# Kernel optimization log

Hardware: AMD Instinct MI355X
Metric: run time of the kernel (lower is better)

The kernel has to match this reference:

```python
import jax, jax.numpy as jnp
import numpy as np

H = 1024
NUM_HEADS = 16
HEAD_DIM = H // NUM_HEADS
EPS = 1e-6
GEN_E, GEN_IE = 8, 4096 // 8     # general experts, per-expert intermediate
MOD_E, MOD_IE = 4, 4096 // 4     # per-modality experts, per-expert intermediate


def layernorm(x, g, b):
    m = jnp.mean(x, axis=-1, keepdims=True)
    v = jnp.mean((x - m) ** 2, axis=-1, keepdims=True)
    return (x - m) * jax.lax.rsqrt(v + EPS) * g + b


def attention(x, qkv_w, qkv_b, proj_w, proj_b):
    B, N, _ = x.shape
    qkv = (x @ qkv_w + qkv_b).reshape(B, N, 3, NUM_HEADS, HEAD_DIM)
    qkv = jnp.transpose(qkv, (2, 0, 3, 1, 4))  # [3,B,h,N,d]
    q, k, v = qkv[0], qkv[1], qkv[2]
    scale = HEAD_DIM ** -0.5
    attn = jax.nn.softmax(jnp.einsum('bhnd,bhmd->bhnm', q, k) * scale, axis=-1)
    out = jnp.einsum('bhnm,bhmd->bhnd', attn, v)
    out = jnp.transpose(out, (0, 2, 1, 3)).reshape(B, N, H)
    return out @ proj_w + proj_b


def routed_mlp(x, position_ids, gate_up, down, ie):
    # expert_id = position % num_experts; compute all experts then select per token
    # (avoids materializing per-token [T,H,2I] gathered weights).
    E = gate_up.shape[0]
    eids = position_ids % E  # [B,N]
    gu = jnp.einsum('bnh,ehi->bnei', x, gate_up)              # [B,N,E,2*ie]
    gu = jnp.take_along_axis(gu, eids[..., None, None], axis=2)[:, :, 0]
    gate, up = gu[..., :ie], gu[..., ie:]
    inter = jax.nn.silu(gate) * up                             # [B,N,ie]
    dn = jnp.einsum('bni,eih->bneh', inter, down)              # [B,N,E,H]
    return jnp.take_along_axis(dn, eids[..., None, None], axis=2)[:, :, 0]


def setup_inputs() -> dict:
    key = jax.random.key(0)
    ks = jax.random.split(key, 16)
    B, N = 2, 2048
    inp = {
        'x': jax.random.normal(ks[0], (B, N, H), jnp.float32),
        'qkv_w': jax.random.normal(ks[1], (H, 3 * H), jnp.float32) * 0.02,
        'qkv_b': jnp.zeros((3 * H,), jnp.float32),
        'proj_w': jax.random.normal(ks[2], (H, H), jnp.float32) * 0.02,
        'proj_b': jnp.zeros((H,), jnp.float32),
        'ln1_g': jnp.ones((H,), jnp.float32), 'ln1_b': jnp.zeros((H,), jnp.float32),
        'ln2_g': jnp.ones((H,), jnp.float32), 'ln2_b': jnp.zeros((H,), jnp.float32),
        'ln3_g': jnp.ones((H,), jnp.float32), 'ln3_b': jnp.zeros((H,), jnp.float32),
        'gen_gu': jax.random.normal(ks[3], (GEN_E, H, 2 * GEN_IE), jnp.float32) * 0.02,
        'gen_dn': jax.random.normal(ks[4], (GEN_E, GEN_IE, H), jnp.float32) * 0.02,
        'text_gu': jax.random.normal(ks[5], (MOD_E, H, 2 * MOD_IE), jnp.float32) * 0.02,
        'text_dn': jax.random.normal(ks[6], (MOD_E, MOD_IE, H), jnp.float32) * 0.02,
        'img_gu': jax.random.normal(ks[7], (MOD_E, H, 2 * MOD_IE), jnp.float32) * 0.02,
        'img_dn': jax.random.normal(ks[8], (MOD_E, MOD_IE, H), jnp.float32) * 0.02,
        'aud_gu': jax.random.normal(ks[9], (MOD_E, H, 2 * MOD_IE), jnp.float32) * 0.02,
        'aud_dn': jax.random.normal(ks[10], (MOD_E, MOD_IE, H), jnp.float32) * 0.02,
        'vid_gu': jax.random.normal(ks[11], (MOD_E, H, 2 * MOD_IE), jnp.float32) * 0.02,
        'vid_dn': jax.random.normal(ks[12], (MOD_E, MOD_IE, H), jnp.float32) * 0.02,
        'modality_ids': jax.random.randint(ks[13], (B, N), 0, 4, jnp.int32),
        'position_ids': jnp.arange(B * N, dtype=jnp.int32).reshape(B, N),
    }
    return inp


def reference(x, qkv_w, qkv_b, proj_w, proj_b,
              ln1_g, ln1_b, ln2_g, ln2_b, ln3_g, ln3_b,
              gen_gu, gen_dn, text_gu, text_dn, img_gu, img_dn,
              aud_gu, aud_dn, vid_gu, vid_dn,
              modality_ids, position_ids):
    x = x + attention(layernorm(x, ln1_g, ln1_b), qkv_w, qkv_b, proj_w, proj_b)
    x = x + routed_mlp(layernorm(x, ln2_g, ln2_b), position_ids, gen_gu, gen_dn, GEN_IE)
    normed = layernorm(x, ln3_g, ln3_b)
    tm = (modality_ids == 0)[..., None].astype(x.dtype)
    im = (modality_ids == 1)[..., None].astype(x.dtype)
    am = (modality_ids == 2)[..., None].astype(x.dtype)
    vm = (modality_ids == 3)[..., None].astype(x.dtype)
    x = x + (routed_mlp(normed, position_ids, text_gu, text_dn, MOD_IE) * tm
             + routed_mlp(normed, position_ids, img_gu, img_dn, MOD_IE) * im
             + routed_mlp(normed, position_ids, aud_gu, aud_dn, MOD_IE) * am
             + routed_mlp(normed, position_ids, vid_gu, vid_dn, MOD_IE) * vm)
    return x
```

## Files before the change

kernel.cpp:

```cpp
#include <hip/hip_runtime.h>

#define T_TOKENS 4096
#define HDIM 1024

typedef __attribute__((ext_vector_type(8))) short bf16x8;
typedef __attribute__((ext_vector_type(4))) float f32x4;

#define EXP2F(x) __builtin_amdgcn_exp2f(x)

static __device__ inline unsigned short f2bf(float f) {
  unsigned u = __float_as_uint(f);
  unsigned r = (u + 0x7FFFu + ((u >> 16) & 1u)) >> 16;
  return (unsigned short)r;
}
static __device__ __forceinline__ unsigned cvtpk(float lo, float hi) {
  unsigned r;
  asm("v_cvt_pk_bf16_f32 %0, %1, %2" : "=v"(r) : "v"(lo), "v"(hi));
  return r;
}
static __device__ __forceinline__ void gl16(const void* g, void* l) {
  __builtin_amdgcn_global_load_lds((const __attribute__((address_space(1))) void*)g,
                                   (__attribute__((address_space(3))) void*)l, 16, 0, 0);
}

__launch_bounds__(256)
__global__ void ln_kernel(const float* __restrict__ in, const float* __restrict__ g,
                          const float* __restrict__ b, unsigned short* __restrict__ out) {
  const int row = blockIdx.x;
  const int tid = threadIdx.x;
  const long base = (long)row * HDIM;
  float4 v = *(const float4*)(in + base + tid * 4);
  __shared__ float red[256];
  red[tid] = v.x + v.y + v.z + v.w;
  __syncthreads();
  for (int st = 128; st > 0; st >>= 1) {
    if (tid < st) red[tid] += red[tid + st];
    __syncthreads();
  }
  const float mean = red[0] * (1.f / HDIM);
  __syncthreads();
  const float dx = v.x - mean, dy = v.y - mean, dz = v.z - mean, dw = v.w - mean;
  red[tid] = dx * dx + dy * dy + dz * dz + dw * dw;
  __syncthreads();
  for (int st = 128; st > 0; st >>= 1) {
    if (tid < st) red[tid] += red[tid + st];
    __syncthreads();
  }
  const float rstd = rsqrtf(red[0] * (1.f / HDIM) + 1e-6f);
  const int c = tid * 4;
  const float4 g4 = *(const float4*)(g + c);
  const float4 b4 = *(const float4*)(b + c);
  uint2 o;
  o.x = cvtpk(dx * rstd * g4.x + b4.x, dy * rstd * g4.y + b4.y);
  o.y = cvtpk(dz * rstd * g4.z + b4.z, dw * rstd * g4.w + b4.w);
  *(uint2*)(out + base + c) = o;
}

__launch_bounds__(256)
__global__ void build_groups(const int* __restrict__ pids, const int* __restrict__ mids,
                             int* __restrict__ gen_cnt, int* __restrict__ gen_list,
                             int* __restrict__ mod_cnt, int* __restrict__ mod_list) {
  const int t = blockIdx.x * 256 + threadIdx.x;
  if (t >= T_TOKENS) return;
  const int p = pids[t];
  const int ge = p & 7;
  int s = atomicAdd(&gen_cnt[ge], 1);
  if (s < 512) gen_list[ge * 512 + s] = t;
  const int g = mids[t] * 4 + (p & 3);
  s = atomicAdd(&mod_cnt[g], 1);
  if (s < 1024) mod_list[g * 1024 + s] = t;
}

__launch_bounds__(256)
__global__ void convert_w(const float* __restrict__ W, unsigned short* __restrict__ Wt,
                          int K, int N) {
  const long zo = (long)blockIdx.z * K * N;
  const float* Wp = W + zo;
  unsigned short* Wo = Wt + zo;
  const int n0 = blockIdx.x * 64, k0 = blockIdx.y * 64;
  __shared__ float T[64][65];
  const int tid = threadIdx.x;
#pragma unroll
  for (int i = 0; i < 4; ++i) {
    const int item = tid + i * 256;
    const int kk = item >> 4, c4 = (item & 15) * 4;
    const float4 v = *(const float4*)(Wp + (long)(k0 + kk) * N + n0 + c4);
    T[c4 + 0][kk] = v.x; T[c4 + 1][kk] = v.y; T[c4 + 2][kk] = v.z; T[c4 + 3][kk] = v.w;
  }
  __syncthreads();
#pragma unroll
  for (int i = 0; i < 4; ++i) {
    const int item = tid + i * 256;
    const int nn = item >> 4, k4 = (item & 15) * 4;
    uint2 p;
    p.x = cvtpk(T[nn][k4 + 0], T[nn][k4 + 1]);
    p.y = cvtpk(T[nn][k4 + 2], T[nn][k4 + 3]);
    *(uint2*)(Wo + (long)(n0 + nn) * K + k0 + k4) = p;
  }
}

enum { MODE_DENSE = 0, MODE_GEN = 1, MODE_MOD = 2 };
enum { OM_F32R = 0, OM_BF16 = 1, OM_QKV = 2 };

template <int MODE, int OMODE, bool WBF16, bool BIAS, int BM, int BN>
__launch_bounds__(256)
__global__ void mgemm(const unsigned short* __restrict__ A,
                      const void* __restrict__ w0, const float* __restrict__ w1,
                      const float* __restrict__ w2, const float* __restrict__ w3,
                      long wstep, const float* __restrict__ bias,
                      const float* __restrict__ resid, void* __restrict__ Cout,
                      unsigned short* __restrict__ qb, unsigned short* __restrict__ kb,
                      unsigned short* __restrict__ vtb,
                      int K, int N,
                      const int* __restrict__ cnts, const int* __restrict__ rowlist,
                      int cap) {
  const int z = blockIdx.z;
  const int n0 = blockIdx.x * BN;
  const int m0 = blockIdx.y * BM;

  int Meff = 1 << 30;
  const int* list = nullptr;
  if constexpr (MODE != MODE_DENSE) {
    Meff = cnts[z];
    if (m0 >= Meff) return;
    list = rowlist + z * cap;
  }

  constexpr int MR = BM / 32;
  constexpr int NR = BN / 32;
  constexpr int JB = BN / 32;
  constexpr int ABUF = BM * 128;
  constexpr int BBUF = BN * 128;
  __shared__ char As[2 * ABUF];
  __shared__ char Bs[2 * BBUF];

  const int tid = threadIdx.x;
  const int w = tid >> 6;
  const int lane = tid & 63;
  const int wm = w >> 1, wn = w & 1;
  const int srow = lane >> 3, sc = lane & 7;

  const unsigned short* asrc[MR];
#pragma unroll
  for (int i = 0; i < MR; ++i) {
    const int r = w * (BM / 4) + i * 8 + srow;
    long tok;
    if constexpr (MODE == MODE_DENSE) {
      tok = m0 + r;
    } else {
      int gm = m0 + r;
      if (gm >= Meff) gm = Meff - 1;
      tok = (long)list[gm];
    }
    asrc[i] = A + tok * (long)K + (sc ^ (r & 7)) * 8;
  }

  const unsigned short* bsrc[NR];
  const float* bptr[JB];
  int boff[JB];
  if constexpr (WBF16) {
    const unsigned short* W = (const unsigned short*)w0;
    if constexpr (MODE != MODE_DENSE) W += (long)z * wstep;
#pragma unroll
    for (int i = 0; i < NR; ++i) {
      const int r = w * (BN / 4) + i * 8 + srow;
      bsrc[i] = W + (long)(n0 + r) * K + (sc ^ (r & 7)) * 8;
    }
  } else {
    const float* W;
    if constexpr (MODE == MODE_MOD) {
      const int mm = z >> 2;
      const float* basep = (mm == 0) ? (const float*)w0 : (mm == 1) ? w1 : (mm == 2) ? w2 : w3;
      W = basep + (long)(z & 3) * wstep;
    } else {
      W = (const float*)w0 + (MODE != MODE_DENSE ? (long)z * wstep : 0);
    }
#pragma unroll
    for (int j = 0; j < JB; ++j) {
      const int item = tid + j * 256;
      const int kc = item / BN;
      const int nl = item % BN;
      bptr[j] = W + (long)(kc * 8) * N + n0 + nl;
      boff[j] = (nl * 128 + kc * 16) ^ ((nl & 7) << 4);
    }
  }

  f32x4 acc[MR][NR] = {};
  float kv[JB][8];

  auto stageA = [&](int s, int kt) {
#pragma unroll
    for (int i = 0; i < MR; ++i)
      gl16(asrc[i] + kt, As + s * ABUF + w * (BM * 32) + i * 1024);
  };
  auto stageB16 = [&](int s, int kt) {
#pragma unroll
    for (int i = 0; i < NR; ++i)
      gl16(bsrc[i] + kt, Bs + s * BBUF + w * (BN * 32) + i * 1024);
  };
  auto loadB = [&](int kt) {
#pragma unroll
    for (int j = 0; j < JB; ++j) {
      const float* bp = bptr[j] + (long)kt * N;
#pragma unroll
      for (int u = 0; u < 8; ++u) kv[j][u] = bp[(long)u * N];
    }
  };
  auto writeB = [&](int s) {
#pragma unroll
    for (int j = 0; j < JB; ++j) {
      uint4 p;
      p.x = cvtpk(kv[j][0], kv[j][1]);
      p.y = cvtpk(kv[j][2], kv[j][3]);
      p.z = cvtpk(kv[j][4], kv[j][5]);
      p.w = cvtpk(kv[j][6], kv[j][7]);
      *(uint4*)(Bs + s * BBUF + boff[j]) = p;
    }
  };
  auto compute = [&](int s) {
#pragma unroll
    for (int kk = 0; kk < 2; ++kk) {
      const int kb2 = kk * 64 + (lane >> 4) * 16;
      bf16x8 af[MR], bfr[NR];
#pragma unroll
      for (int f = 0; f < MR; ++f) {
        const int ar = wm * (BM / 2) + f * 16 + (lane & 15);
        af[f] = *(bf16x8*)(As + s * ABUF + ((ar * 128 + kb2) ^ ((ar & 7) << 4)));
      }
#pragma unroll
      for (int f = 0; f < NR; ++f) {
        const int br = wn * (BN / 2) + f * 16 + (lane & 15);
        bfr[f] = *(bf16x8*)(Bs + s * BBUF + ((br * 128 + kb2) ^ ((br & 7) << 4)));
      }
#pragma unroll
      for (int mf = 0; mf < MR; ++mf)
#pragma unroll
        for (int nf = 0; nf < NR; ++nf)
          acc[mf][nf] =
              __builtin_amdgcn_mfma_f32_16x16x32_bf16(af[mf], bfr[nf], acc[mf][nf], 0, 0, 0);
    }
  };

  const int nk = K >> 6;
  stageA(0, 0);
  if constexpr (WBF16) {
    stageB16(0, 0);
  } else {
    loadB(0);
    writeB(0);
  }
  __syncthreads();

  int sel = 0;
  for (int t = 0; t < nk; ++t) {
    const bool more = (t + 1) < nk;
    const int ktn = (t + 1) * 64;
    if (more) {
      stageA(sel ^ 1, ktn);
      if constexpr (WBF16) stageB16(sel ^ 1, ktn);
      else loadB(ktn);
    }
    compute(sel);
    if constexpr (!WBF16) {
      if (more) writeB(sel ^ 1);
    }
    __syncthreads();
    sel ^= 1;
  }

  const int lr4 = (lane >> 4) * 4;
  const int lc = lane & 15;
#pragma unroll
  for (int mf = 0; mf < MR; ++mf) {
#pragma unroll
    for (int r = 0; r < 4; ++r) {
      const int gm = m0 + wm * (BM / 2) + mf * 16 + lr4 + r;
      long orow;
      if constexpr (MODE == MODE_DENSE) {
        orow = gm;
      } else {
        if (gm >= Meff) continue;
        orow = (long)list[gm];
      }
#pragma unroll
      for (int nf = 0; nf < NR; ++nf) {
        const int gc = n0 + wn * (BN / 2) + nf * 16 + lc;
        float val = acc[mf][nf][r];
        if constexpr (BIAS) val += bias[gc];
        if constexpr (OMODE == OM_F32R) {
          val += resid[orow * (long)N + gc];
          ((float*)Cout)[orow * (long)N + gc] = val;
        } else if constexpr (OMODE == OM_BF16) {
          ((unsigned short*)Cout)[orow * (long)N + gc] = f2bf(val);
        } else {
          const int bb = (int)(orow >> 11), tl = (int)orow & 2047;
          const int seg = gc >> 10, hc = gc & 1023, h = hc >> 6, d = hc & 63;
          if (seg == 0)
            qb[(((long)(bb * 16 + h) * 2048) + tl) * 64 + d] = f2bf(val * 0.18033688011112042f);
          else if (seg == 1)
            kb[(((long)(bb * 16 + h) * 2048) + tl) * 64 + d] = f2bf(val);
          else
            vtb[((long)(bb * 16 + h) * 64 + d) * 2048 + tl] = f2bf(val);
        }
      }
    }
  }
}

__launch_bounds__(256)
__global__ void attn_kernel(const unsigned short* __restrict__ Qb,
                            const unsigned short* __restrict__ Kb,
                            const unsigned short* __restrict__ Vtb,
                            unsigned short* __restrict__ out) {
  const int lin = blockIdx.x + blockIdx.y * 32;
  const int xcd = lin & 7, rank = lin >> 3;
  const int bh = xcd * 4 + (rank >> 5);
  const int qt = rank & 31;
  const int b = bh >> 4, h = bh & 15;
  const int tid = threadIdx.x;
  const int w = tid >> 6;
  const int lane = tid & 63;
  const int g = lane >> 4;
  const int q = lane & 15;

  constexpr int PSTR = 272;
  __shared__ char Ksb[128 * 128];
  __shared__ char Vsb[64 * 256];
  __shared__ char Psb[4 * 16 * PSTR];
  char* Pwb = Psb + w * 16 * PSTR;

  const unsigned short* Qh = Qb + ((long)(b * 16 + h) * 2048 + qt * 64) * 64;
  const unsigned short* Kh = Kb + (long)(b * 16 + h) * 2048 * 64;
  const unsigned short* Vh = Vtb + (long)(b * 16 + h) * 64 * 2048;

  bf16x8 qf[2];
#pragma unroll
  for (int kst = 0; kst < 2; ++kst)
    qf[kst] = *(const bf16x8*)(Qh + (w * 16 + q) * 64 + kst * 32 + g * 8);

  const unsigned short* ksrc[4];
  const unsigned short* vsrc[4];
  char* kld = Ksb + w * 4096;
  char* vld = Vsb + w * 4096;
#pragma unroll
  for (int i = 0; i < 4; ++i) {
    const int r = w * 32 + i * 8 + (lane >> 3);
    ksrc[i] = Kh + (long)r * 64 + ((lane & 7) ^ (r & 7)) * 8;
    const int d = w * 16 + i * 4 + (lane >> 4);
    vsrc[i] = Vh + (long)d * 2048 + ((lane & 15) ^ (d & 7)) * 8;
  }

  float m_run = -1e30f, l_run = 0.f;
  f32x4 acc[4] = {};

  for (int kt = 0; kt < 16; ++kt) {
    __syncthreads();
#pragma unroll
    for (int i = 0; i < 4; ++i) gl16(ksrc[i] + (long)kt * 128 * 64, kld + i * 1024);
#pragma unroll
    for (int i = 0; i < 4; ++i) gl16(vsrc[i] + kt * 128, vld + i * 1024);
    __syncthreads();

    f32x4 sf[8];
#pragma unroll
    for (int f = 0; f < 8; ++f) {
      const int krow = f * 16 + q;
      const int sw = (krow & 7) << 4;
      const bf16x8 k0 = *(bf16x8*)(Ksb + krow * 128 + ((g * 16) ^ sw));
      const bf16x8 k1 = *(bf16x8*)(Ksb + krow * 128 + ((64 + g * 16) ^ sw));
      f32x4 t = {};
      t = __builtin_amdgcn_mfma_f32_16x16x32_bf16(k0, qf[0], t, 0, 0, 0);
      sf[f] = __builtin_amdgcn_mfma_f32_16x16x32_bf16(k1, qf[1], t, 0, 0, 0);
    }

    float pm = fmaxf(fmaxf(sf[0][0], sf[0][1]), fmaxf(sf[0][2], sf[0][3]));
#pragma unroll
    for (int f = 1; f < 8; ++f)
      pm = fmaxf(pm, fmaxf(fmaxf(sf[f][0], sf[f][1]), fmaxf(sf[f][2], sf[f][3])));
    pm = fmaxf(pm, __shfl_xor(pm, 16));
    pm = fmaxf(pm, __shfl_xor(pm, 32));
    float al = 1.f;
    if (!__all(pm - m_run <= 8.f)) {
      const float mn = fmaxf(m_run, pm);
      al = EXP2F(m_run - mn);
      m_run = mn;
#pragma unroll
      for (int r = 0; r < 4; ++r) {
        const float aO = __shfl(al, g * 4 + r, 64);
        acc[0][r] *= aO; acc[1][r] *= aO; acc[2][r] *= aO; acc[3][r] *= aO;
      }
    }

    float ls = 0.f;
#pragma unroll
    for (int f = 0; f < 8; ++f) {
#pragma unroll
      for (int r = 0; r < 4; ++r) sf[f][r] = EXP2F(sf[f][r] - m_run);
      ls += (sf[f][0] + sf[f][1]) + (sf[f][2] + sf[f][3]);
    }
    ls += __shfl_xor(ls, 16);
    ls += __shfl_xor(ls, 32);
    l_run = l_run * al + ls;

#pragma unroll
    for (int f = 0; f < 8; ++f) {
      const int base = q * PSTR + f * 32 + g * 8;
      *(unsigned*)(Pwb + base) = cvtpk(sf[f][0], sf[f][1]);
      *(unsigned*)(Pwb + base + 4) = cvtpk(sf[f][2], sf[f][3]);
    }

#pragma unroll
    for (int kst = 0; kst < 4; ++kst) {
      const bf16x8 pa = *(bf16x8*)(Pwb + q * PSTR + kst * 64 + g * 16);
#pragma unroll
      for (int df = 0; df < 4; ++df) {
        const int vrow = df * 16 + q;
        const int vsw = (vrow & 7) << 4;
        const bf16x8 vf = *(bf16x8*)(Vsb + vrow * 256 + ((kst * 64 + g * 16) ^ vsw));
        acc[df] = __builtin_amdgcn_mfma_f32_16x16x32_bf16(pa, vf, acc[df], 0, 0, 0);
      }
    }
  }

  float linv[4];
#pragma unroll
  for (int r = 0; r < 4; ++r) linv[r] = 1.f / __shfl(l_run, g * 4 + r, 64);
  unsigned short* op = out + (long)(b * 2048 + qt * 64 + w * 16) * 1024 + h * 64;
#pragma unroll
  for (int df = 0; df < 4; ++df)
#pragma unroll
    for (int r = 0; r < 4; ++r) {
      const int row = g * 4 + r;
      op[(long)row * 1024 + df * 16 + q] = f2bf(acc[df][r] * linv[r]);
    }
}

__launch_bounds__(256)
__global__ void silu_bf(const unsigned short* __restrict__ gu, unsigned short* __restrict__ inter,
                        int IE2, int IE, int shift) {
  const int total = T_TOKENS << shift;
  for (int idx = blockIdx.x * 256 + threadIdx.x; idx < total; idx += gridDim.x * 256) {
    const int t = idx >> shift;
    const int r8 = (idx & ((1 << shift) - 1)) * 8;
    const unsigned short* gp = gu + (long)t * IE2 + r8;
    const uint4 gg = *(const uint4*)gp;
    const uint4 uu = *(const uint4*)(gp + IE);
    const unsigned gw[4] = {gg.x, gg.y, gg.z, gg.w};
    const unsigned uw[4] = {uu.x, uu.y, uu.z, uu.w};
    uint4 o;
    unsigned ow[4];
#pragma unroll
    for (int qq = 0; qq < 4; ++qq) {
      const float g0 = __uint_as_float(gw[qq] << 16);
      const float g1 = __uint_as_float(gw[qq] & 0xffff0000u);
      const float u0 = __uint_as_float(uw[qq] << 16);
      const float u1 = __uint_as_float(uw[qq] & 0xffff0000u);
      const float r0 = g0 / (1.f + __expf(-g0)) * u0;
      const float r1 = g1 / (1.f + __expf(-g1)) * u1;
      ow[qq] = cvtpk(r0, r1);
    }
    o.x = ow[0]; o.y = ow[1]; o.z = ow[2]; o.w = ow[3];
    *(uint4*)(inter + (long)t * IE + r8) = o;
  }
}

extern "C" void kernel_launch(void* const* d_in, const int* in_sizes, int n_in,
                              void* d_out, int out_size, void* d_ws, size_t ws_size,
                              hipStream_t stream) {
  const float* x       = (const float*)d_in[0];
  const float* qkv_w   = (const float*)d_in[1];
  const float* qkv_b   = (const float*)d_in[2];
  const float* proj_w  = (const float*)d_in[3];
  const float* proj_b  = (const float*)d_in[4];
  const float* ln1_g   = (const float*)d_in[5];
  const float* ln1_b   = (const float*)d_in[6];
  const float* ln2_g   = (const float*)d_in[7];
  const float* ln2_b   = (const float*)d_in[8];
  const float* ln3_g   = (const float*)d_in[9];
  const float* ln3_b   = (const float*)d_in[10];
  const float* gen_gu  = (const float*)d_in[11];
  const float* gen_dn  = (const float*)d_in[12];
  const float* text_gu = (const float*)d_in[13];
  const float* text_dn = (const float*)d_in[14];
  const float* img_gu  = (const float*)d_in[15];
  const float* img_dn  = (const float*)d_in[16];
  const float* aud_gu  = (const float*)d_in[17];
  const float* aud_dn  = (const float*)d_in[18];
  const float* vid_gu  = (const float*)d_in[19];
  const float* vid_dn  = (const float*)d_in[20];
  const int* mids      = (const int*)d_in[21];
  const int* pids      = (const int*)d_in[22];
  float* out = (float*)d_out;
  char* ws = (char*)d_ws;

  const unsigned long MB = 1ul << 20;
  unsigned short* lnb   = (unsigned short*)(ws);
  unsigned short* Qb    = (unsigned short*)(ws + 8 * MB);
  unsigned short* Kb    = (unsigned short*)(ws + 16 * MB);
  unsigned short* Vtb   = (unsigned short*)(ws + 24 * MB);
  unsigned short* attno = (unsigned short*)(ws + 32 * MB);
  unsigned short* wqkv  = (unsigned short*)(ws + 40 * MB);
  unsigned short* wproj = (unsigned short*)(ws + 46 * MB);
  unsigned short* wggu  = (unsigned short*)(ws + 48 * MB);
  unsigned short* wgdn  = (unsigned short*)(ws + 64 * MB);
  int* gen_cnt  = (int*)(ws + 72 * MB);
  int* mod_cnt  = gen_cnt + 8;
  int* gen_list = gen_cnt + 32;
  int* mod_list = gen_list + 8 * 512;
  unsigned short* guo    = Qb;
  unsigned short* intero = Vtb;

  (void)hipMemsetAsync(gen_cnt, 0, (8 + 16) * sizeof(int), stream);
  build_groups<<<16, 256, 0, stream>>>(pids, mids, gen_cnt, gen_list, mod_cnt, mod_list);

  convert_w<<<dim3(48, 16, 1), 256, 0, stream>>>(qkv_w, wqkv, 1024, 3072);
  convert_w<<<dim3(16, 16, 1), 256, 0, stream>>>(proj_w, wproj, 1024, 1024);
  convert_w<<<dim3(16, 16, 8), 256, 0, stream>>>(gen_gu, wggu, 1024, 1024);
  convert_w<<<dim3(16, 8, 8), 256, 0, stream>>>(gen_dn, wgdn, 512, 1024);

  ln_kernel<<<4096, 256, 0, stream>>>(x, ln1_g, ln1_b, lnb);
  mgemm<MODE_DENSE, OM_QKV, true, true, 128, 128><<<dim3(24, 32, 1), 256, 0, stream>>>(
      lnb, wqkv, nullptr, nullptr, nullptr, 0L, qkv_b, nullptr, nullptr,
      Qb, Kb, Vtb, 1024, 3072, nullptr, nullptr, 0);
  attn_kernel<<<dim3(32, 32, 1), 256, 0, stream>>>(Qb, Kb, Vtb, attno);
  mgemm<MODE_DENSE, OM_F32R, true, true, 128, 128><<<dim3(8, 32, 1), 256, 0, stream>>>(
      attno, wproj, nullptr, nullptr, nullptr, 0L, proj_b, x, out,
      nullptr, nullptr, nullptr, 1024, 1024, nullptr, nullptr, 0);

  ln_kernel<<<4096, 256, 0, stream>>>(out, ln2_g, ln2_b, lnb);
  mgemm<MODE_GEN, OM_BF16, true, false, 128, 128><<<dim3(8, 4, 8), 256, 0, stream>>>(
      lnb, wggu, nullptr, nullptr, nullptr, (long)1024 * 1024, nullptr, nullptr, guo,
      nullptr, nullptr, nullptr, 1024, 1024, gen_cnt, gen_list, 512);
  silu_bf<<<1024, 256, 0, stream>>>(guo, intero, 1024, 512, 6);
  mgemm<MODE_GEN, OM_F32R, true, false, 128, 128><<<dim3(8, 4, 8), 256, 0, stream>>>(
      intero, wgdn, nullptr, nullptr, nullptr, (long)1024 * 512, nullptr, out, out,
      nullptr, nullptr, nullptr, 512, 1024, gen_cnt, gen_list, 512);

  ln_kernel<<<4096, 256, 0, stream>>>(out, ln3_g, ln3_b, lnb);
  mgemm<MODE_MOD, OM_BF16, false, false, 128, 64><<<dim3(32, 8, 16), 256, 0, stream>>>(
      lnb, text_gu, img_gu, aud_gu, vid_gu, (long)1024 * 2048, nullptr, nullptr, guo,
      nullptr, nullptr, nullptr, 1024, 2048, mod_cnt, mod_list, 1024);
  silu_bf<<<2048, 256, 0, stream>>>(guo, intero, 2048, 1024, 7);
  mgemm<MODE_MOD, OM_F32R, false, false, 128, 64><<<dim3(16, 8, 16), 256, 0, stream>>>(
      intero, text_dn, img_dn, aud_dn, vid_dn, (long)1024 * 1024, nullptr, out, out,
      nullptr, nullptr, nullptr, 1024, 1024, mod_cnt, mod_list, 1024);
}
```

Measured before the change: 384.5 us.

## Double per-warp query rows in attention and widen modality MLP GEMM tiles

The attention kernel now has each block cover 128 query rows instead of 64, with each warp handling two 16-row query tiles (A and B). Every K/V tile loaded into LDS is therefore reused across twice as many queries, and the grid is halved. The P staging buffer switches from a padded stride to an XOR-swizzled 256-byte stride. Separately, the modality gate/up and down GEMMs move from 128x64 to 128x128 tiles. The trade-off is more registers per thread, which may lower occupancy, plus fewer blocks across the GPU.

```diff
diff --git a/kernel.cpp b/kernel.cpp
--- a/kernel.cpp
+++ b/kernel.cpp
@@ -312,10 +312,10 @@
                             const unsigned short* __restrict__ Kb,
                             const unsigned short* __restrict__ Vtb,
                             unsigned short* __restrict__ out) {
-  const int lin = blockIdx.x + blockIdx.y * 32;
+  const int lin = blockIdx.x + blockIdx.y * 16;
   const int xcd = lin & 7, rank = lin >> 3;
-  const int bh = xcd * 4 + (rank >> 5);
-  const int qt = rank & 31;
+  const int bh = xcd * 4 + (rank >> 4);
+  const int qt = rank & 15;
   const int b = bh >> 4, h = bh & 15;
   const int tid = threadIdx.x;
   const int w = tid >> 6;
@@ -323,20 +323,22 @@
   const int g = lane >> 4;
   const int q = lane & 15;
 
-  constexpr int PSTR = 272;
   __shared__ char Ksb[128 * 128];
   __shared__ char Vsb[64 * 256];
-  __shared__ char Psb[4 * 16 * PSTR];
-  char* Pwb = Psb + w * 16 * PSTR;
-
-  const unsigned short* Qh = Qb + ((long)(b * 16 + h) * 2048 + qt * 64) * 64;
+  __shared__ char Psb[4 * 32 * 256];
+  char* Pwb = Psb + w * 32 * 256;
+  const int qx = q << 4;
+
+  const unsigned short* Qh = Qb + ((long)(b * 16 + h) * 2048 + qt * 128) * 64;
   const unsigned short* Kh = Kb + (long)(b * 16 + h) * 2048 * 64;
   const unsigned short* Vh = Vtb + (long)(b * 16 + h) * 64 * 2048;
 
-  bf16x8 qf[2];
-#pragma unroll
-  for (int kst = 0; kst < 2; ++kst)
-    qf[kst] = *(const bf16x8*)(Qh + (w * 16 + q) * 64 + kst * 32 + g * 8);
+  bf16x8 qfA[2], qfB[2];
+#pragma unroll
+  for (int kst = 0; kst < 2; ++kst) {
+    qfA[kst] = *(const bf16x8*)(Qh + (w * 32 + q) * 64 + kst * 32 + g * 8);
+    qfB[kst] = *(const bf16x8*)(Qh + (w * 32 + 16 + q) * 64 + kst * 32 + g * 8);
+  }
 
   const unsigned short* ksrc[4];
   const unsigned short* vsrc[4];
@@ -350,8 +352,8 @@
     vsrc[i] = Vh + (long)d * 2048 + ((lane & 15) ^ (d & 7)) * 8;
   }
 
-  float m_run = -1e30f, l_run = 0.f;
-  f32x4 acc[4] = {};
+  float mA = -1e30f, lA = 0.f, mB = -1e30f, lB = 0.f;
+  f32x4 accA[4] = {}, accB[4] = {};
 
   for (int kt = 0; kt < 16; ++kt) {
     __syncthreads();
@@ -361,77 +363,120 @@
     for (int i = 0; i < 4; ++i) gl16(vsrc[i] + kt * 128, vld + i * 1024);
     __syncthreads();
 
-    f32x4 sf[8];
+    f32x4 sfA[8], sfB[8];
 #pragma unroll
     for (int f = 0; f < 8; ++f) {
       const int krow = f * 16 + q;
       const int sw = (krow & 7) << 4;
       const bf16x8 k0 = *(bf16x8*)(Ksb + krow * 128 + ((g * 16) ^ sw));
       const bf16x8 k1 = *(bf16x8*)(Ksb + krow * 128 + ((64 + g * 16) ^ sw));
-      f32x4 t = {};
-      t = __builtin_amdgcn_mfma_f32_16x16x32_bf16(k0, qf[0], t, 0, 0, 0);
-      sf[f] = __builtin_amdgcn_mfma_f32_16x16x32_bf16(k1, qf[1], t, 0, 0, 0);
-    }
-
-    float pm = fmaxf(fmaxf(sf[0][0], sf[0][1]), fmaxf(sf[0][2], sf[0][3]));
-#pragma unroll
-    for (int f = 1; f < 8; ++f)
-      pm = fmaxf(pm, fmaxf(fmaxf(sf[f][0], sf[f][1]), fmaxf(sf[f][2], sf[f][3])));
-    pm = fmaxf(pm, __shfl_xor(pm, 16));
-    pm = fmaxf(pm, __shfl_xor(pm, 32));
-    float al = 1.f;
-    if (!__all(pm - m_run <= 8.f)) {
-      const float mn = fmaxf(m_run, pm);
-      al = EXP2F(m_run - mn);
-      m_run = mn;
-#pragma unroll
-      for (int r = 0; r < 4; ++r) {
-        const float aO = __shfl(al, g * 4 + r, 64);
-        acc[0][r] *= aO; acc[1][r] *= aO; acc[2][r] *= aO; acc[3][r] *= aO;
-      }
-    }
-
-    float ls = 0.f;
+      f32x4 tA = {};
+      tA = __builtin_amdgcn_mfma_f32_16x16x32_bf16(k0, qfA[0], tA, 0, 0, 0);
+      sfA[f] = __builtin_amdgcn_mfma_f32_16x16x32_bf16(k1, qfA[1], tA, 0, 0, 0);
+      f32x4 tB = {};
+      tB = __builtin_amdgcn_mfma_f32_16x16x32_bf16(k0, qfB[0], tB, 0, 0, 0);
+      sfB[f] = __builtin_amdgcn_mfma_f32_16x16x32_bf16(k1, qfB[1], tB, 0, 0, 0);
+    }
+
+    {
+      float pm = fmaxf(fmaxf(sfA[0][0], sfA[0][1]), fmaxf(sfA[0][2], sfA[0][3]));
+#pragma unroll
+      for (int f = 1; f < 8; ++f)
+        pm = fmaxf(pm, fmaxf(fmaxf(sfA[f][0], sfA[f][1]), fmaxf(sfA[f][2], sfA[f][3])));
+      pm = fmaxf(pm, __shfl_xor(pm, 16));
+      pm = fmaxf(pm, __shfl_xor(pm, 32));
+      float al = 1.f;
+      if (!__all(pm - mA <= 8.f)) {
+        const float mn = fmaxf(mA, pm);
+        al = EXP2F(mA - mn);
+        mA = mn;
+#pragma unroll
+        for (int r = 0; r < 4; ++r) {
+          const float aO = __shfl(al, g * 4 + r, 64);
+          accA[0][r] *= aO; accA[1][r] *= aO; accA[2][r] *= aO; accA[3][r] *= aO;
+        }
+      }
+      float ls = 0.f;
+#pragma unroll
+      for (int f = 0; f < 8; ++f) {
+#pragma unroll
+        for (int r = 0; r < 4; ++r) sfA[f][r] = EXP2F(sfA[f][r] - mA);
+        ls += (sfA[f][0] + sfA[f][1]) + (sfA[f][2] + sfA[f][3]);
+      }
+      ls += __shfl_xor(ls, 16);
+      ls += __shfl_xor(ls, 32);
+      lA = lA * al + ls;
+    }
+    {
+      float pm = fmaxf(fmaxf(sfB[0][0], sfB[0][1]), fmaxf(sfB[0][2], sfB[0][3]));
+#pragma unroll
+      for (int f = 1; f < 8; ++f)
+        pm = fmaxf(pm, fmaxf(fmaxf(sfB[f][0], sfB[f][1]), fmaxf(sfB[f][2], sfB[f][3])));
+      pm = fmaxf(pm, __shfl_xor(pm, 16));
+      pm = fmaxf(pm, __shfl_xor(pm, 32));
+      float al = 1.f;
+      if (!__all(pm - mB <= 8.f)) {
+        const float mn = fmaxf(mB, pm);
+        al = EXP2F(mB - mn);
+        mB = mn;
+#pragma unroll
+        for (int r = 0; r < 4; ++r) {
+          const float aO = __shfl(al, g * 4 + r, 64);
+          accB[0][r] *= aO; accB[1][r] *= aO; accB[2][r] *= aO; accB[3][r] *= aO;
+        }
+      }
+      float ls = 0.f;
+#pragma unroll
+      for (int f = 0; f < 8; ++f) {
+#pragma unroll
+        for (int r = 0; r < 4; ++r) sfB[f][r] = EXP2F(sfB[f][r] - mB);
+        ls += (sfB[f][0] + sfB[f][1]) + (sfB[f][2] + sfB[f][3]);
+      }
+      ls += __shfl_xor(ls, 16);
+      ls += __shfl_xor(ls, 32);
+      lB = lB * al + ls;
+    }
+
 #pragma unroll
     for (int f = 0; f < 8; ++f) {
-#pragma unroll
-      for (int r = 0; r < 4; ++r) sf[f][r] = EXP2F(sf[f][r] - m_run);
-      ls += (sf[f][0] + sf[f][1]) + (sf[f][2] + sf[f][3]);
-    }
-    ls += __shfl_xor(ls, 16);
-    ls += __shfl_xor(ls, 32);
-    l_run = l_run * al + ls;
-
-#pragma unroll
-    for (int f = 0; f < 8; ++f) {
-      const int base = q * PSTR + f * 32 + g * 8;
-      *(unsigned*)(Pwb + base) = cvtpk(sf[f][0], sf[f][1]);
-      *(unsigned*)(Pwb + base + 4) = cvtpk(sf[f][2], sf[f][3]);
+      const int col = (f * 32 + g * 8) ^ qx;
+      uint2 pA; pA.x = cvtpk(sfA[f][0], sfA[f][1]); pA.y = cvtpk(sfA[f][2], sfA[f][3]);
+      *(uint2*)(Pwb + q * 256 + col) = pA;
+      uint2 pB; pB.x = cvtpk(sfB[f][0], sfB[f][1]); pB.y = cvtpk(sfB[f][2], sfB[f][3]);
+      *(uint2*)(Pwb + (q + 16) * 256 + col) = pB;
     }
 
 #pragma unroll
     for (int kst = 0; kst < 4; ++kst) {
-      const bf16x8 pa = *(bf16x8*)(Pwb + q * PSTR + kst * 64 + g * 16);
+      const int pcol = (kst * 64 + g * 16) ^ qx;
+      const bf16x8 paA = *(bf16x8*)(Pwb + q * 256 + pcol);
+      const bf16x8 paB = *(bf16x8*)(Pwb + (q + 16) * 256 + pcol);
 #pragma unroll
       for (int df = 0; df < 4; ++df) {
         const int vrow = df * 16 + q;
         const int vsw = (vrow & 7) << 4;
         const bf16x8 vf = *(bf16x8*)(Vsb + vrow * 256 + ((kst * 64 + g * 16) ^ vsw));
-        acc[df] = __builtin_amdgcn_mfma_f32_16x16x32_bf16(pa, vf, acc[df], 0, 0, 0);
-      }
-    }
-  }
-
-  float linv[4];
-#pragma unroll
-  for (int r = 0; r < 4; ++r) linv[r] = 1.f / __shfl(l_run, g * 4 + r, 64);
-  unsigned short* op = out + (long)(b * 2048 + qt * 64 + w * 16) * 1024 + h * 64;
+        accA[df] = __builtin_amdgcn_mfma_f32_16x16x32_bf16(paA, vf, accA[df], 0, 0, 0);
+        accB[df] = __builtin_amdgcn_mfma_f32_16x16x32_bf16(paB, vf, accB[df], 0, 0, 0);
+      }
+    }
+  }
+
+  float liA[4], liB[4];
+#pragma unroll
+  for (int r = 0; r < 4; ++r) {
+    liA[r] = 1.f / __shfl(lA, g * 4 + r, 64);
+    liB[r] = 1.f / __shfl(lB, g * 4 + r, 64);
+  }
+  unsigned short* opA = out + (long)(b * 2048 + qt * 128 + w * 32) * 1024 + h * 64;
+  unsigned short* opB = opA + 16 * 1024;
 #pragma unroll
   for (int df = 0; df < 4; ++df)
 #pragma unroll
     for (int r = 0; r < 4; ++r) {
       const int row = g * 4 + r;
-      op[(long)row * 1024 + df * 16 + q] = f2bf(acc[df][r] * linv[r]);
+      opA[(long)row * 1024 + df * 16 + q] = f2bf(accA[df][r] * liA[r]);
+      opB[(long)row * 1024 + df * 16 + q] = f2bf(accB[df][r] * liB[r]);
     }
 }
 
@@ -522,7 +567,7 @@
   mgemm<MODE_DENSE, OM_QKV, true, true, 128, 128><<<dim3(24, 32, 1), 256, 0, stream>>>(
       lnb, wqkv, nullptr, nullptr, nullptr, 0L, qkv_b, nullptr, nullptr,
       Qb, Kb, Vtb, 1024, 3072, nullptr, nullptr, 0);
-  attn_kernel<<<dim3(32, 32, 1), 256, 0, stream>>>(Qb, Kb, Vtb, attno);
+  attn_kernel<<<dim3(16, 32, 1), 256, 0, stream>>>(Qb, Kb, Vtb, attno);
   mgemm<MODE_DENSE, OM_F32R, true, true, 128, 128><<<dim3(8, 32, 1), 256, 0, stream>>>(
       attno, wproj, nullptr, nullptr, nullptr, 0L, proj_b, x, out,
       nullptr, nullptr, nullptr, 1024, 1024, nullptr, nullptr, 0);
@@ -537,11 +582,11 @@
       nullptr, nullptr, nullptr, 512, 1024, gen_cnt, gen_list, 512);
 
   ln_kernel<<<4096, 256, 0, stream>>>(out, ln3_g, ln3_b, lnb);
-  mgemm<MODE_MOD, OM_BF16, false, false, 128, 64><<<dim3(32, 8, 16), 256, 0, stream>>>(
+  mgemm<MODE_MOD, OM_BF16, false, false, 128, 128><<<dim3(16, 8, 16), 256, 0, stream>>>(
       lnb, text_gu, img_gu, aud_gu, vid_gu, (long)1024 * 2048, nullptr, nullptr, guo,
       nullptr, nullptr, nullptr, 1024, 2048, mod_cnt, mod_list, 1024);
   silu_bf<<<2048, 256, 0, stream>>>(guo, intero, 2048, 1024, 7);
-  mgemm<MODE_MOD, OM_F32R, false, false, 128, 64><<<dim3(16, 8, 16), 256, 0, stream>>>(
+  mgemm<MODE_MOD, OM_F32R, false, false, 128, 128><<<dim3(8, 8, 16), 256, 0, stream>>>(
       intero, text_dn, img_dn, aud_dn, vid_dn, (long)1024 * 1024, nullptr, out, out,
       nullptr, nullptr, nullptr, 1024, 1024, mod_cnt, mod_list, 1024);
 }
```

Result: no change. 388.2 us (+1.0%).
